# Optimization experiments

Measured on AMD Instinct MI355X. Metric: run time of the kernel, lower is better.

## Reference

```python
import jax, jax.numpy as jnp
import numpy as np

NEG = -1e9  # stand-in for -inf mask fill (avoids NaN, softmax weight ~0)
EPS = 1e-5  # torch LayerNorm default


def layer_norm(x, g, b):
    mu = jnp.mean(x, axis=-1, keepdims=True)
    var = jnp.mean(jnp.square(x - mu), axis=-1, keepdims=True)
    return (x - mu) * jax.lax.rsqrt(var + EPS) * g + b


def _forward(x, context, batch_lengths, max_len,
             Wq1, Wk1, Wv1, Wq2, Wk2, Wv2,
             ln1_g, ln1_b, ln2_g, ln2_b, ln3_g, ln3_b,
             fc1_w, fc1_b, fc2_w, fc2_b):
    B, L, E = x.shape
    H, _, dk = Wq1.shape
    pos = jnp.arange(L)
    valid = pos[None, :] < batch_lengths[:, None]                  # [B,L]
    out_mask = valid[:, :, None].astype(x.dtype)                   # [B,L,1] (outputMask)
    key_bias = jnp.where(valid, 0.0, NEG)[:, None, None, :]        # [B,1,1,L] (attnMask on keys)
    causal_bias = jnp.where(pos[:, None] >= pos[None, :], 0.0, NEG)  # [L,L] decoding mask
    scale = 1.0 / jnp.sqrt(jnp.asarray(dk, x.dtype))

    def mha(qk_src, v_src, Wq, Wk, Wv, causal):
        # Q,K from qk_src, V from v_src (faithful to Head.forward)
        m = out_mask[:, None]                                      # [B,1,L,1]
        Q = jnp.einsum('ble,hed->bhld', qk_src, Wq) * m
        K = jnp.einsum('ble,hed->bhld', qk_src, Wk) * m
        V = jnp.einsum('ble,hed->bhld', v_src, Wv) * m
        e = jnp.einsum('bhid,bhjd->bhij', Q, K) + key_bias
        if causal:
            e = e + causal_bias
        s = jax.nn.softmax(e * scale, axis=-1)
        o = jnp.einsum('bhij,bhjd->bhid', s, V)
        return o.transpose(0, 2, 1, 3).reshape(B, L, E)            # concat heads

    z = mha(x, x, Wq1, Wk1, Wv1, causal=True) * out_mask
    x1 = layer_norm(x + z, ln1_g, ln1_b)
    # cross block: Q,K from context, V from x1 (as in source)
    z = mha(context, x1, Wq2, Wk2, Wv2, causal=False) * out_mask
    x2 = layer_norm(x1 + z, ln2_g, ln2_b)
    h = jax.nn.relu(x2 @ fc1_w + fc1_b) * out_mask
    z = (h @ fc2_w + fc2_b) * out_mask
    return layer_norm(x2 + z, ln3_g, ln3_b)


def setup_inputs() -> dict:
    B, L, E, H = 8, 1024, 1024, 16
    dk = E // H
    key = jax.random.key(0)
    ks = jax.random.split(key, 16)
    w = lambda k, s: jax.random.normal(k, s, jnp.float32) * 0.02
    return {
        'x': jax.random.normal(ks[0], (B, L, E), jnp.float32),
        'context': jax.random.normal(ks[1], (B, L, E), jnp.float32),
        'batch_lengths': jax.random.randint(ks[2], (B,), 1, L + 1),
        'max_len': L,
        'Wq1': w(ks[3], (H, E, dk)), 'Wk1': w(ks[4], (H, E, dk)), 'Wv1': w(ks[5], (H, E, dk)),
        'Wq2': w(ks[6], (H, E, dk)), 'Wk2': w(ks[7], (H, E, dk)), 'Wv2': w(ks[8], (H, E, dk)),
        'ln1_g': jnp.ones((E,), jnp.float32), 'ln1_b': jnp.zeros((E,), jnp.float32),
        'ln2_g': jnp.ones((E,), jnp.float32), 'ln2_b': jnp.zeros((E,), jnp.float32),
        'ln3_g': jnp.ones((E,), jnp.float32), 'ln3_b': jnp.zeros((E,), jnp.float32),
        'fc1_w': w(ks[9], (E, E)), 'fc1_b': jnp.zeros((E,), jnp.float32),
        'fc2_w': w(ks[10], (E, E)), 'fc2_b': jnp.zeros((E,), jnp.float32),
    }


def reference(x, context, batch_lengths, max_len,
              Wq1, Wk1, Wv1, Wq2, Wk2, Wv2,
              ln1_g, ln1_b, ln2_g, ln2_b, ln3_g, ln3_b,
              fc1_w, fc1_b, fc2_w, fc2_b):
    return _forward(x, context, batch_lengths, max_len,
                    Wq1, Wk1, Wv1, Wq2, Wk2, Wv2,
                    ln1_g, ln1_b, ln2_g, ln2_b, ln3_g, ln3_b,
                    fc1_w, fc1_b, fc2_w, fc2_b)
```

## Files before the change

### kernel.cpp

```cpp
#include <hip/hip_runtime.h>


typedef unsigned short u16;
typedef unsigned int u32;
typedef __attribute__((ext_vector_type(8))) short bf16x8;
typedef __attribute__((ext_vector_type(4))) float f32x4;

#define Bv 8
#define Lv 1024
#define Ev 1024
#define Hv 16
#define DKv 64
#define Mv (Bv * Lv)

__device__ __forceinline__ u16 f2bf(float f) {
    u32 u = __float_as_uint(f);
    u += 0x7fffu + ((u >> 16) & 1u);
    return (u16)(u >> 16);
}
__device__ __forceinline__ u32 pack2(float a, float b) {
    u32 ua = __float_as_uint(a); ua += 0x7fffu + ((ua >> 16) & 1u);
    u32 ub = __float_as_uint(b); ub += 0x7fffu + ((ub >> 16) & 1u);
    return (ua >> 16) | (ub & 0xffff0000u);
}

__global__ __launch_bounds__(256) void conv_k(const float* __restrict__ s, u16* __restrict__ d) {
    int i4 = (blockIdx.x * 256 + threadIdx.x) * 4;
    float4 v = *(const float4*)(s + i4);
    uint2 o = {pack2(v.x, v.y), pack2(v.z, v.w)};
    *(uint2*)(d + i4) = o;
}

__global__ __launch_bounds__(256) void trans_attn(const float* __restrict__ s, u16* __restrict__ d) {
    __shared__ float t[32][33];
    const int d0 = blockIdx.x * 32, e0 = blockIdx.y * 32, h = blockIdx.z;
    const int tx = threadIdx.x, ty = threadIdx.y;
#pragma unroll
    for (int i = 0; i < 4; i++)
        t[ty + i * 8][tx] = s[(size_t)h * Ev * DKv + (size_t)(e0 + ty + i * 8) * DKv + d0 + tx];
    __syncthreads();
#pragma unroll
    for (int i = 0; i < 4; i++)
        d[(size_t)(h * DKv + d0 + ty + i * 8) * Ev + e0 + tx] = f2bf(t[tx][ty + i * 8]);
}

__global__ __launch_bounds__(256) void trans_fc(const float* __restrict__ s, u16* __restrict__ d) {
    __shared__ float t[32][33];
    const int n0 = blockIdx.x * 32, k0 = blockIdx.y * 32;
    const int tx = threadIdx.x, ty = threadIdx.y;
#pragma unroll
    for (int i = 0; i < 4; i++)
        t[ty + i * 8][tx] = s[(size_t)(k0 + ty + i * 8) * Ev + n0 + tx];
    __syncthreads();
#pragma unroll
    for (int i = 0; i < 4; i++)
        d[(size_t)(n0 + ty + i * 8) * Ev + k0 + tx] = f2bf(t[tx][ty + i * 8]);
}

template <int BIAS, int RELU, int TRANSOUT>
__global__ __launch_bounds__(256) void mgemm(const u16* __restrict__ A,
                                             const u16* __restrict__ Wt,
                                             const float* __restrict__ bias,
                                             u16* __restrict__ C,
                                             const int* __restrict__ lens) {
    __shared__ u16 Alds[16 * 520];
    __shared__ u16 Blds[16 * 520];
    const int tid = threadIdx.x;
    const int w = tid >> 6, l = tid & 63;
    const int lc = l & 15, lq = l >> 4;
    const int row0 = blockIdx.y * 128, col0 = blockIdx.x * 128;
    const int wm4 = (w >> 1) * 4, wn4 = (w & 1) * 4;

    f32x4 acc[4][4];
#pragma unroll
    for (int i = 0; i < 4; i++)
#pragma unroll
        for (int j = 0; j < 4; j++) acc[i][j] = (f32x4){0.f, 0.f, 0.f, 0.f};

    for (int k0 = 0; k0 < Ev; k0 += 64) {
        const u16* Ag = A + (size_t)row0 * Ev + k0;
        const u16* Bg = Wt + (size_t)col0 * Ev + k0;
#pragma unroll
        for (int i = 0; i < 4; i++) {
            int s = i * 256 + tid;
            int row = s >> 3, g = s & 7;
            uint4 va = *(const uint4*)(Ag + (size_t)row * Ev + g * 8);
            uint4 vb = *(const uint4*)(Bg + (size_t)row * Ev + g * 8);
            int off = ((row >> 4) * 2 + (g >> 2)) * 520 + ((g & 3) * 16 + (row & 15)) * 8;
            *(uint4*)(Alds + off) = va;
            *(uint4*)(Blds + off) = vb;
        }
        __syncthreads();
#pragma unroll
        for (int km = 0; km < 2; km++) {
            bf16x8 af[4], bfr[4];
#pragma unroll
            for (int mt = 0; mt < 4; mt++)
                af[mt] = *(const bf16x8*)(Alds + ((wm4 + mt) * 2 + km) * 520 + l * 8);
#pragma unroll
            for (int nt = 0; nt < 4; nt++)
                bfr[nt] = *(const bf16x8*)(Blds + ((wn4 + nt) * 2 + km) * 520 + l * 8);
#pragma unroll
            for (int mt = 0; mt < 4; mt++)
#pragma unroll
                for (int nt = 0; nt < 4; nt++)
                    acc[mt][nt] = __builtin_amdgcn_mfma_f32_16x16x32_bf16(
                        af[mt], bfr[nt], acc[mt][nt], 0, 0, 0);
        }
        __syncthreads();
    }

    int len = lens[row0 >> 10];
    len = min(max(len, 0), Lv);
    float bv[4];
#pragma unroll
    for (int nt = 0; nt < 4; nt++)
        bv[nt] = BIAS ? bias[col0 + wn4 * 16 + nt * 16 + lc] : 0.f;

#pragma unroll
    for (int mt = 0; mt < 4; mt++) {
        const int rowb = row0 + wm4 * 16 + mt * 16 + lq * 4;
#pragma unroll
        for (int nt = 0; nt < 4; nt++) {
            const int col = col0 + wn4 * 16 + nt * 16 + lc;
            float v[4];
#pragma unroll
            for (int r = 0; r < 4; r++) {
                float x = acc[mt][nt][r] + bv[nt];
                if (RELU) x = fmaxf(x, 0.f);
                v[r] = (((rowb + r) & (Lv - 1)) >= len) ? 0.f : x;
            }
            if (TRANSOUT) {
                uint2 o = {pack2(v[0], v[1]), pack2(v[2], v[3])};
                *(uint2*)(C + (size_t)col * Mv + rowb) = o;
            } else {
#pragma unroll
                for (int r = 0; r < 4; r++)
                    C[(size_t)(rowb + r) * Ev + col] = f2bf(v[r]);
            }
        }
    }
}

template <int CAUSAL>
__global__ __launch_bounds__(256) void mattn(u16* __restrict__ QZ,
                                             const u16* __restrict__ K,
                                             const u16* __restrict__ VT,
                                             const int* __restrict__ lens) {
    __shared__ u16 Kt[128 * 72];
    __shared__ u16 Vt[64 * 136];
    __shared__ u16 Pw[4 * 16 * 136];
    const int b = blockIdx.z, h = blockIdx.y, qb = blockIdx.x;
    const int q0 = qb * 64;
    const int tid = threadIdx.x;
    const int w = tid >> 6, l = tid & 63;
    const int lc = l & 15, lq = l >> 4;
    int len = lens[b];
    len = min(max(len, 0), Lv);

    if (q0 >= len) {
        const int row = q0 + (tid >> 2), cc = (tid & 3) * 16;
        uint4 z4 = {0u, 0u, 0u, 0u};
        uint4* p = (uint4*)(QZ + (size_t)(b * Lv + row) * Ev + h * DKv + cc);
        p[0] = z4; p[1] = z4;
        return;
    }

    const size_t qrow = (size_t)(b * Lv + q0 + w * 16 + lc) * Ev + h * DKv;
    bf16x8 qf[2];
    qf[0] = *(const bf16x8*)(QZ + qrow + lq * 8);
    qf[1] = *(const bf16x8*)(QZ + qrow + 32 + lq * 8);

    f32x4 of[4];
#pragma unroll
    for (int i = 0; i < 4; i++) of[i] = (f32x4){0.f, 0.f, 0.f, 0.f};
    float mrow[4] = {-1e30f, -1e30f, -1e30f, -1e30f};
    float lrow[4] = {0.f, 0.f, 0.f, 0.f};

    const int jend = CAUSAL ? min(len, q0 + 64) : len;
    const int ntiles = (jend + 127) >> 7;

    for (int kt = 0; kt < ntiles; kt++) {
        const int key0 = kt * 128;
        __syncthreads();
        {
            const u16* kg = K + (size_t)(b * Lv + key0 + (tid & 127)) * Ev + h * DKv + (tid >> 7) * 32;
            u16* kd = Kt + (tid & 127) * 72 + (tid >> 7) * 32;
#pragma unroll
            for (int c = 0; c < 4; c++) *(uint4*)(kd + c * 8) = *(const uint4*)(kg + c * 8);
            const u16* vg = VT + (size_t)(h * DKv + (tid >> 2)) * Mv + b * Lv + key0 + (tid & 3) * 32;
            u16* vd = Vt + (tid >> 2) * 136 + (tid & 3) * 32;
#pragma unroll
            for (int c = 0; c < 4; c++) *(uint4*)(vd + c * 8) = *(const uint4*)(vg + c * 8);
        }
        __syncthreads();

        f32x4 sf[8];
#pragma unroll
        for (int nt = 0; nt < 8; nt++) {
            bf16x8 b0 = *(const bf16x8*)(Kt + (nt * 16 + lc) * 72 + lq * 8);
            bf16x8 b1 = *(const bf16x8*)(Kt + (nt * 16 + lc) * 72 + 32 + lq * 8);
            f32x4 s = (f32x4){0.f, 0.f, 0.f, 0.f};
            s = __builtin_amdgcn_mfma_f32_16x16x32_bf16(qf[0], b0, s, 0, 0, 0);
            s = __builtin_amdgcn_mfma_f32_16x16x32_bf16(qf[1], b1, s, 0, 0, 0);
            sf[nt] = s;
        }
        float tmax[4] = {-1e30f, -1e30f, -1e30f, -1e30f};
#pragma unroll
        for (int nt = 0; nt < 8; nt++) {
            const int jj = key0 + nt * 16 + lc;
            const bool jv = jj < len;
#pragma unroll
            for (int r = 0; r < 4; r++) {
                const int iq = q0 + w * 16 + lq * 4 + r;
                const bool valid = jv && (!CAUSAL || jj <= iq);
                float e = valid ? sf[nt][r] * 0.125f : -1e30f;
                sf[nt][r] = e;
                tmax[r] = fmaxf(tmax[r], e);
            }
        }
#pragma unroll
        for (int r = 0; r < 4; r++) {
#pragma unroll
            for (int d = 1; d < 16; d <<= 1)
                tmax[r] = fmaxf(tmax[r], __shfl_xor(tmax[r], d, 64));
        }
        float alpha[4], mnew[4], psum[4];
#pragma unroll
        for (int r = 0; r < 4; r++) {
            mnew[r] = fmaxf(mrow[r], tmax[r]);
            alpha[r] = __expf(mrow[r] - mnew[r]);
            psum[r] = 0.f;
        }
#pragma unroll
        for (int nt = 0; nt < 8; nt++)
#pragma unroll
            for (int r = 0; r < 4; r++) {
                float p = __expf(sf[nt][r] - mnew[r]);
                sf[nt][r] = p;
                psum[r] += p;
            }
#pragma unroll
        for (int r = 0; r < 4; r++) {
#pragma unroll
            for (int d = 1; d < 16; d <<= 1) psum[r] += __shfl_xor(psum[r], d, 64);
            lrow[r] = lrow[r] * alpha[r] + psum[r];
            mrow[r] = mnew[r];
        }
#pragma unroll
        for (int nd = 0; nd < 4; nd++)
#pragma unroll
            for (int r = 0; r < 4; r++) of[nd][r] *= alpha[r];
        u16* pw = Pw + w * (16 * 136);
#pragma unroll
        for (int nt = 0; nt < 8; nt++)
#pragma unroll
            for (int r = 0; r < 4; r++)
                pw[(lq * 4 + r) * 136 + nt * 16 + lc] = f2bf(sf[nt][r]);
#pragma unroll
        for (int nd = 0; nd < 4; nd++) {
#pragma unroll
            for (int km = 0; km < 4; km++) {
                bf16x8 pa = *(const bf16x8*)(pw + lc * 136 + km * 32 + lq * 8);
                bf16x8 vb = *(const bf16x8*)(Vt + (nd * 16 + lc) * 136 + km * 32 + lq * 8);
                of[nd] = __builtin_amdgcn_mfma_f32_16x16x32_bf16(pa, vb, of[nd], 0, 0, 0);
            }
        }
    }

    float inv[4];
#pragma unroll
    for (int r = 0; r < 4; r++) {
        const int iq = q0 + w * 16 + lq * 4 + r;
        inv[r] = (iq < len && lrow[r] > 0.f) ? (1.f / lrow[r]) : 0.f;
    }
#pragma unroll
    for (int nd = 0; nd < 4; nd++)
#pragma unroll
        for (int r = 0; r < 4; r++)
            QZ[(size_t)(b * Lv + q0 + w * 16 + lq * 4 + r) * Ev + h * DKv + nd * 16 + lc] =
                f2bf(of[nd][r] * inv[r]);
}

__device__ __forceinline__ float bf_lo(u32 u) { return __uint_as_float(u << 16); }
__device__ __forceinline__ float bf_hi(u32 u) { return __uint_as_float(u & 0xffff0000u); }

template <int BASEBF, int OUTF32>
__global__ __launch_bounds__(256) void ln_k(const void* __restrict__ base,
                                            const u16* __restrict__ z,
                                            const float* __restrict__ g,
                                            const float* __restrict__ bta,
                                            void* __restrict__ out) {
    __shared__ float r1[256], r2[256];
    const int row = blockIdx.x, t = threadIdx.x;
    const int c0 = t * 4;
    float v[4];
    if (BASEBF) {
        uint2 bu = *(const uint2*)((const u16*)base + (size_t)row * Ev + c0);
        v[0] = bf_lo(bu.x); v[1] = bf_hi(bu.x); v[2] = bf_lo(bu.y); v[3] = bf_hi(bu.y);
    } else {
        float4 f = *(const float4*)((const float*)base + (size_t)row * Ev + c0);
        v[0] = f.x; v[1] = f.y; v[2] = f.z; v[3] = f.w;
    }
    uint2 zu = *(const uint2*)(z + (size_t)row * Ev + c0);
    v[0] += bf_lo(zu.x); v[1] += bf_hi(zu.x); v[2] += bf_lo(zu.y); v[3] += bf_hi(zu.y);
    r1[t] = v[0] + v[1] + v[2] + v[3];
    r2[t] = v[0] * v[0] + v[1] * v[1] + v[2] * v[2] + v[3] * v[3];
    __syncthreads();
    for (int s = 128; s > 0; s >>= 1) {
        if (t < s) { r1[t] += r1[t + s]; r2[t] += r2[t + s]; }
        __syncthreads();
    }
    const float mu = r1[0] * (1.f / Ev);
    const float var = r2[0] * (1.f / Ev) - mu * mu;
    const float rinv = rsqrtf(fmaxf(var, 0.f) + 1e-5f);
    float4 gv = *(const float4*)(g + c0);
    float4 bv = *(const float4*)(bta + c0);
    float y[4];
    y[0] = (v[0] - mu) * rinv * gv.x + bv.x;
    y[1] = (v[1] - mu) * rinv * gv.y + bv.y;
    y[2] = (v[2] - mu) * rinv * gv.z + bv.z;
    y[3] = (v[3] - mu) * rinv * gv.w + bv.w;
    if (OUTF32) {
        float4 ow = {y[0], y[1], y[2], y[3]};
        *(float4*)((float*)out + (size_t)row * Ev + c0) = ow;
    } else {
        uint2 ow = {pack2(y[0], y[1]), pack2(y[2], y[3])};
        *(uint2*)((u16*)out + (size_t)row * Ev + c0) = ow;
    }
}

extern "C" void kernel_launch(void* const* d_in, const int* in_sizes, int n_in,
                              void* d_out, int out_size, void* d_ws, size_t ws_size,
                              hipStream_t stream) {
    const float* x    = (const float*)d_in[0];
    const float* ctx  = (const float*)d_in[1];
    const int*   lens = (const int*)d_in[2];
    const float* Wq1 = (const float*)d_in[4];
    const float* Wk1 = (const float*)d_in[5];
    const float* Wv1 = (const float*)d_in[6];
    const float* Wq2 = (const float*)d_in[7];
    const float* Wk2 = (const float*)d_in[8];
    const float* Wv2 = (const float*)d_in[9];
    const float* g1 = (const float*)d_in[10], *b1 = (const float*)d_in[11];
    const float* g2 = (const float*)d_in[12], *b2 = (const float*)d_in[13];
    const float* g3 = (const float*)d_in[14], *b3 = (const float*)d_in[15];
    const float* fc1w = (const float*)d_in[16], *fc1b = (const float*)d_in[17];
    const float* fc2w = (const float*)d_in[18], *fc2b = (const float*)d_in[19];

    const size_t WSZ = (size_t)Ev * Ev;
    const size_t MM  = (size_t)Mv * Ev;
    u16* WT = (u16*)d_ws;
    u16* Wtq1 = WT + 0 * WSZ, *Wtk1 = WT + 1 * WSZ, *Wtv1 = WT + 2 * WSZ;
    u16* Wtq2 = WT + 3 * WSZ, *Wtk2 = WT + 4 * WSZ, *Wtv2 = WT + 5 * WSZ;
    u16* Wtf1 = WT + 6 * WSZ, *Wtf2 = WT + 7 * WSZ;
    u16* B1 = WT + 8 * WSZ;
    u16* B2 = B1 + MM;
    u16* B3 = B2 + MM;
    u16* B4 = B3 + MM;
    u16* xb = (u16*)d_out;
    u16* cb = xb + MM;

    dim3 gC(Mv * Ev / 1024), gTA(2, 32, Hv), gTF(32, 32), bT(32, 8);
    dim3 gG(8, 64), gA(16, Hv, Bv), gL(Mv);

    conv_k<<<gC, 256, 0, stream>>>(x, xb);
    conv_k<<<gC, 256, 0, stream>>>(ctx, cb);
    trans_attn<<<gTA, bT, 0, stream>>>(Wq1, Wtq1);
    trans_attn<<<gTA, bT, 0, stream>>>(Wk1, Wtk1);
    trans_attn<<<gTA, bT, 0, stream>>>(Wv1, Wtv1);
    trans_attn<<<gTA, bT, 0, stream>>>(Wq2, Wtq2);
    trans_attn<<<gTA, bT, 0, stream>>>(Wk2, Wtk2);
    trans_attn<<<gTA, bT, 0, stream>>>(Wv2, Wtv2);
    trans_fc<<<gTF, bT, 0, stream>>>(fc1w, Wtf1);
    trans_fc<<<gTF, bT, 0, stream>>>(fc2w, Wtf2);

    mgemm<0, 0, 0><<<gG, 256, 0, stream>>>(xb, Wtq1, nullptr, B1, lens);
    mgemm<0, 0, 0><<<gG, 256, 0, stream>>>(xb, Wtk1, nullptr, B2, lens);
    mgemm<0, 0, 1><<<gG, 256, 0, stream>>>(xb, Wtv1, nullptr, B3, lens);
    mattn<1><<<gA, 256, 0, stream>>>(B1, B2, B3, lens);
    ln_k<0, 0><<<gL, 256, 0, stream>>>(x, B1, g1, b1, B2);

    mgemm<0, 0, 0><<<gG, 256, 0, stream>>>(cb, Wtq2, nullptr, B1, lens);
    mgemm<0, 0, 0><<<gG, 256, 0, stream>>>(cb, Wtk2, nullptr, B3, lens);
    mgemm<0, 0, 1><<<gG, 256, 0, stream>>>(B2, Wtv2, nullptr, B4, lens);
    mattn<0><<<gA, 256, 0, stream>>>(B1, B3, B4, lens);
    ln_k<1, 0><<<gL, 256, 0, stream>>>(B2, B1, g2, b2, B3);

    mgemm<1, 1, 0><<<gG, 256, 0, stream>>>(B3, Wtf1, fc1b, B1, lens);
    mgemm<1, 0, 0><<<gG, 256, 0, stream>>>(B1, Wtf2, fc2b, B4, lens);
    ln_k<1, 1><<<gL, 256, 0, stream>>>(B3, B4, g3, b3, d_out);
}
```

Before: 566.7 us.

## Fuse QKV projections, use direct global-to-LDS loads, enlarge attention query tile

```diff
diff --git a/kernel.cpp b/kernel.cpp
--- a/kernel.cpp
+++ b/kernel.cpp
@@ -13,6 +13,24 @@
 #define DKv 64
 #define Mv (Bv * Lv)
 
+#if defined(__has_builtin)
+# if __has_builtin(__builtin_amdgcn_global_load_lds)
+#  define HAS_GLL 1
+# endif
+#endif
+#ifndef HAS_GLL
+# define HAS_GLL 0
+#endif
+
+#if HAS_GLL
+__device__ __forceinline__ void gll16(const u16* g, u16* l) {
+    __builtin_amdgcn_global_load_lds(
+        (const __attribute__((address_space(1))) void*)(unsigned long long)(g),
+        (__attribute__((address_space(3))) void*)(unsigned)(unsigned long long)(l),
+        16, 0, 0);
+}
+#endif
+
 __device__ __forceinline__ u16 f2bf(float f) {
     u32 u = __float_as_uint(f);
     u += 0x7fffu + ((u >> 16) & 1u);
@@ -23,6 +41,8 @@
     u32 ub = __float_as_uint(b); ub += 0x7fffu + ((ub >> 16) & 1u);
     return (ua >> 16) | (ub & 0xffff0000u);
 }
+__device__ __forceinline__ float bf_lo(u32 u) { return __uint_as_float(u << 16); }
+__device__ __forceinline__ float bf_hi(u32 u) { return __uint_as_float(u & 0xffff0000u); }
 
 __global__ __launch_bounds__(256) void conv_k(const float* __restrict__ s, u16* __restrict__ d) {
     int i4 = (blockIdx.x * 256 + threadIdx.x) * 4;
@@ -57,18 +77,21 @@
         d[(size_t)(n0 + ty + i * 8) * Ev + k0 + tx] = f2bf(t[tx][ty + i * 8]);
 }
 
-template <int BIAS, int RELU, int TRANSOUT>
+template <int BIAS, int RELU, int TRANSW>
 __global__ __launch_bounds__(256) void mgemm(const u16* __restrict__ A,
                                              const u16* __restrict__ Wt,
                                              const float* __restrict__ bias,
-                                             u16* __restrict__ C,
+                                             u16* __restrict__ O0, u16* __restrict__ O1,
+                                             u16* __restrict__ O2,
                                              const int* __restrict__ lens) {
-    __shared__ u16 Alds[16 * 520];
-    __shared__ u16 Blds[16 * 520];
+    __shared__ u16 Alds[16 * 512];
+    __shared__ u16 Blds[16 * 512];
     const int tid = threadIdx.x;
     const int w = tid >> 6, l = tid & 63;
     const int lc = l & 15, lq = l >> 4;
     const int row0 = blockIdx.y * 128, col0 = blockIdx.x * 128;
+    const int which = col0 >> 10, colL = col0 & 1023;
+    u16* C = (which == 0) ? O0 : (which == 1 ? O1 : O2);
     const int wm4 = (w >> 1) * 4, wn4 = (w & 1) * 4;
 
     f32x4 acc[4][4];
@@ -77,29 +100,39 @@
 #pragma unroll
         for (int j = 0; j < 4; j++) acc[i][j] = (f32x4){0.f, 0.f, 0.f, 0.f};
 
+    const u16* Ag[4]; const u16* Bg[4]; u16* Al[4]; u16* Bl[4];
+#pragma unroll
+    for (int i = 0; i < 4; i++) {
+        const int g16 = 2 * w + (i >> 1), k32 = i & 1;
+        Ag[i] = A  + (size_t)(row0 + g16 * 16 + lc) * Ev + k32 * 32 + lq * 8;
+        Bg[i] = Wt + (size_t)(col0 + g16 * 16 + lc) * Ev + k32 * 32 + lq * 8;
+        Al[i] = Alds + (g16 * 2 + k32) * 512;
+        Bl[i] = Blds + (g16 * 2 + k32) * 512;
+    }
+
     for (int k0 = 0; k0 < Ev; k0 += 64) {
-        const u16* Ag = A + (size_t)row0 * Ev + k0;
-        const u16* Bg = Wt + (size_t)col0 * Ev + k0;
+#if HAS_GLL
+#pragma unroll
+        for (int i = 0; i < 4; i++) { gll16(Ag[i], Al[i]); gll16(Bg[i], Bl[i]); }
+#else
 #pragma unroll
         for (int i = 0; i < 4; i++) {
-            int s = i * 256 + tid;
-            int row = s >> 3, g = s & 7;
-            uint4 va = *(const uint4*)(Ag + (size_t)row * Ev + g * 8);
-            uint4 vb = *(const uint4*)(Bg + (size_t)row * Ev + g * 8);
-            int off = ((row >> 4) * 2 + (g >> 2)) * 520 + ((g & 3) * 16 + (row & 15)) * 8;
-            *(uint4*)(Alds + off) = va;
-            *(uint4*)(Blds + off) = vb;
-        }
+            *(uint4*)(Al[i] + l * 8) = *(const uint4*)Ag[i];
+            *(uint4*)(Bl[i] + l * 8) = *(const uint4*)Bg[i];
+        }
+#endif
+#pragma unroll
+        for (int i = 0; i < 4; i++) { Ag[i] += 64; Bg[i] += 64; }
         __syncthreads();
 #pragma unroll
         for (int km = 0; km < 2; km++) {
             bf16x8 af[4], bfr[4];
 #pragma unroll
             for (int mt = 0; mt < 4; mt++)
-                af[mt] = *(const bf16x8*)(Alds + ((wm4 + mt) * 2 + km) * 520 + l * 8);
+                af[mt] = *(const bf16x8*)(Alds + ((wm4 + mt) * 2 + km) * 512 + l * 8);
 #pragma unroll
             for (int nt = 0; nt < 4; nt++)
-                bfr[nt] = *(const bf16x8*)(Blds + ((wn4 + nt) * 2 + km) * 520 + l * 8);
+                bfr[nt] = *(const bf16x8*)(Blds + ((wn4 + nt) * 2 + km) * 512 + l * 8);
 #pragma unroll
             for (int mt = 0; mt < 4; mt++)
 #pragma unroll
@@ -112,17 +145,18 @@
 
     int len = lens[row0 >> 10];
     len = min(max(len, 0), Lv);
+    const bool tr = (TRANSW == which);
     float bv[4];
 #pragma unroll
     for (int nt = 0; nt < 4; nt++)
-        bv[nt] = BIAS ? bias[col0 + wn4 * 16 + nt * 16 + lc] : 0.f;
+        bv[nt] = BIAS ? bias[colL + wn4 * 16 + nt * 16 + lc] : 0.f;
 
 #pragma unroll
     for (int mt = 0; mt < 4; mt++) {
         const int rowb = row0 + wm4 * 16 + mt * 16 + lq * 4;
 #pragma unroll
         for (int nt = 0; nt < 4; nt++) {
-            const int col = col0 + wn4 * 16 + nt * 16 + lc;
+            const int col = colL + wn4 * 16 + nt * 16 + lc;
             float v[4];
 #pragma unroll
             for (int r = 0; r < 4; r++) {
@@ -130,7 +164,7 @@
                 if (RELU) x = fmaxf(x, 0.f);
                 v[r] = (((rowb + r) & (Lv - 1)) >= len) ? 0.f : x;
             }
-            if (TRANSOUT) {
+            if (tr) {
                 uint2 o = {pack2(v[0], v[1]), pack2(v[2], v[3])};
                 *(uint2*)(C + (size_t)col * Mv + rowb) = o;
             } else {
@@ -147,11 +181,11 @@
                                              const u16* __restrict__ K,
                                              const u16* __restrict__ VT,
                                              const int* __restrict__ lens) {
-    __shared__ u16 Kt[128 * 72];
-    __shared__ u16 Vt[64 * 136];
-    __shared__ u16 Pw[4 * 16 * 136];
+    __shared__ u16 Kt[16 * 512];
+    __shared__ u16 Vt[16 * 512];
+    __shared__ u16 Pt[4 * 4 * 512];
     const int b = blockIdx.z, h = blockIdx.y, qb = blockIdx.x;
-    const int q0 = qb * 64;
+    const int q0 = qb * 128;
     const int tid = threadIdx.x;
     const int w = tid >> 6, l = tid & 63;
     const int lc = l & 15, lq = l >> 4;
@@ -159,131 +193,166 @@
     len = min(max(len, 0), Lv);
 
     if (q0 >= len) {
-        const int row = q0 + (tid >> 2), cc = (tid & 3) * 16;
+        const int zr = tid >> 1, zc = (tid & 1) * 32;
         uint4 z4 = {0u, 0u, 0u, 0u};
-        uint4* p = (uint4*)(QZ + (size_t)(b * Lv + row) * Ev + h * DKv + cc);
-        p[0] = z4; p[1] = z4;
+        uint4* p = (uint4*)(QZ + (size_t)(b * Lv + q0 + zr) * Ev + h * DKv + zc);
+        p[0] = z4; p[1] = z4; p[2] = z4; p[3] = z4;
         return;
     }
 
-    const size_t qrow = (size_t)(b * Lv + q0 + w * 16 + lc) * Ev + h * DKv;
-    bf16x8 qf[2];
-    qf[0] = *(const bf16x8*)(QZ + qrow + lq * 8);
-    qf[1] = *(const bf16x8*)(QZ + qrow + 32 + lq * 8);
-
-    f32x4 of[4];
-#pragma unroll
-    for (int i = 0; i < 4; i++) of[i] = (f32x4){0.f, 0.f, 0.f, 0.f};
-    float mrow[4] = {-1e30f, -1e30f, -1e30f, -1e30f};
-    float lrow[4] = {0.f, 0.f, 0.f, 0.f};
-
-    const int jend = CAUSAL ? min(len, q0 + 64) : len;
+    bf16x8 qf[2][2];
+#pragma unroll
+    for (int mt = 0; mt < 2; mt++)
+#pragma unroll
+        for (int k2 = 0; k2 < 2; k2++)
+            qf[mt][k2] = *(const bf16x8*)(QZ + (size_t)(b * Lv + q0 + w * 32 + mt * 16 + lc) * Ev +
+                                          h * DKv + k2 * 32 + lq * 8);
+
+    f32x4 of[2][4];
+#pragma unroll
+    for (int mt = 0; mt < 2; mt++)
+#pragma unroll
+        for (int nd = 0; nd < 4; nd++) of[mt][nd] = (f32x4){0.f, 0.f, 0.f, 0.f};
+    float mrow[2][4], lrow[2][4];
+#pragma unroll
+    for (int mt = 0; mt < 2; mt++)
+#pragma unroll
+        for (int r = 0; r < 4; r++) { mrow[mt][r] = -1e30f; lrow[mt][r] = 0.f; }
+
+    const u16* Kg[4]; const u16* Vg[4]; u16* Kl[4]; u16* Vl[4];
+#pragma unroll
+    for (int i = 0; i < 4; i++) {
+        const int k16 = 2 * w + (i >> 1), d32 = i & 1;
+        Kg[i] = K + (size_t)(b * Lv + k16 * 16 + lc) * Ev + h * DKv + d32 * 32 + lq * 8;
+        Kl[i] = Kt + (k16 * 2 + d32) * 512;
+        Vg[i] = VT + (size_t)(h * DKv + w * 16 + lc) * Mv + b * Lv + i * 32 + lq * 8;
+        Vl[i] = Vt + (w * 4 + i) * 512;
+    }
+    u16* Pw = Pt + w * 2048;
+
+    const int jend = CAUSAL ? min(len, q0 + 128) : len;
     const int ntiles = (jend + 127) >> 7;
 
     for (int kt = 0; kt < ntiles; kt++) {
-        const int key0 = kt * 128;
+        const int koff = kt * 128;
+#if HAS_GLL
+#pragma unroll
+        for (int i = 0; i < 4; i++) {
+            gll16(Kg[i] + (size_t)koff * Ev, Kl[i]);
+            gll16(Vg[i] + koff, Vl[i]);
+        }
+#else
+#pragma unroll
+        for (int i = 0; i < 4; i++) {
+            *(uint4*)(Kl[i] + l * 8) = *(const uint4*)(Kg[i] + (size_t)koff * Ev);
+            *(uint4*)(Vl[i] + l * 8) = *(const uint4*)(Vg[i] + koff);
+        }
+#endif
         __syncthreads();
-        {
-            const u16* kg = K + (size_t)(b * Lv + key0 + (tid & 127)) * Ev + h * DKv + (tid >> 7) * 32;
-            u16* kd = Kt + (tid & 127) * 72 + (tid >> 7) * 32;
-#pragma unroll
-            for (int c = 0; c < 4; c++) *(uint4*)(kd + c * 8) = *(const uint4*)(kg + c * 8);
-            const u16* vg = VT + (size_t)(h * DKv + (tid >> 2)) * Mv + b * Lv + key0 + (tid & 3) * 32;
-            u16* vd = Vt + (tid >> 2) * 136 + (tid & 3) * 32;
-#pragma unroll
-            for (int c = 0; c < 4; c++) *(uint4*)(vd + c * 8) = *(const uint4*)(vg + c * 8);
+
+        f32x4 sf[2][8];
+#pragma unroll
+        for (int nt = 0; nt < 8; nt++) {
+            bf16x8 kf0 = *(const bf16x8*)(Kt + (nt * 2 + 0) * 512 + l * 8);
+            bf16x8 kf1 = *(const bf16x8*)(Kt + (nt * 2 + 1) * 512 + l * 8);
+#pragma unroll
+            for (int mt = 0; mt < 2; mt++) {
+                f32x4 s = (f32x4){0.f, 0.f, 0.f, 0.f};
+                s = __builtin_amdgcn_mfma_f32_16x16x32_bf16(qf[mt][0], kf0, s, 0, 0, 0);
+                s = __builtin_amdgcn_mfma_f32_16x16x32_bf16(qf[mt][1], kf1, s, 0, 0, 0);
+                sf[mt][nt] = s;
+            }
+        }
+
+        float alpha[2][4];
+#pragma unroll
+        for (int mt = 0; mt < 2; mt++) {
+            float tmax[4] = {-1e30f, -1e30f, -1e30f, -1e30f};
+#pragma unroll
+            for (int nt = 0; nt < 8; nt++) {
+                const int jj = koff + nt * 16 + lc;
+                const bool jv = jj < len;
+#pragma unroll
+                for (int r = 0; r < 4; r++) {
+                    const int iq = q0 + w * 32 + mt * 16 + lq * 4 + r;
+                    const bool valid = jv && (!CAUSAL || jj <= iq);
+                    float e = valid ? sf[mt][nt][r] * 0.125f : -1e30f;
+                    sf[mt][nt][r] = e;
+                    tmax[r] = fmaxf(tmax[r], e);
+                }
+            }
+#pragma unroll
+            for (int r = 0; r < 4; r++) {
+#pragma unroll
+                for (int d = 1; d < 16; d <<= 1)
+                    tmax[r] = fmaxf(tmax[r], __shfl_xor(tmax[r], d, 64));
+            }
+            float psum[4];
+#pragma unroll
+            for (int r = 0; r < 4; r++) {
+                const float mn = fmaxf(mrow[mt][r], tmax[r]);
+                alpha[mt][r] = __expf(mrow[mt][r] - mn);
+                mrow[mt][r] = mn;
+                psum[r] = 0.f;
+            }
+#pragma unroll
+            for (int nt = 0; nt < 8; nt++)
+#pragma unroll
+                for (int r = 0; r < 4; r++) {
+                    float p = __expf(sf[mt][nt][r] - mrow[mt][r]);
+                    sf[mt][nt][r] = p;
+                    psum[r] += p;
+                }
+#pragma unroll
+            for (int r = 0; r < 4; r++) {
+#pragma unroll
+                for (int d = 1; d < 16; d <<= 1) psum[r] += __shfl_xor(psum[r], d, 64);
+                lrow[mt][r] = lrow[mt][r] * alpha[mt][r] + psum[r];
+            }
+#pragma unroll
+            for (int nd = 0; nd < 4; nd++)
+#pragma unroll
+                for (int r = 0; r < 4; r++) of[mt][nd][r] *= alpha[mt][r];
+        }
+
+#pragma unroll
+        for (int mt = 0; mt < 2; mt++) {
+#pragma unroll
+            for (int nt = 0; nt < 8; nt++)
+#pragma unroll
+                for (int r = 0; r < 4; r++)
+                    Pw[(nt >> 1) * 512 +
+                       ((2 * (nt & 1) + (lc >> 3)) * 16 + lq * 4 + r) * 8 + (lc & 7)] =
+                        f2bf(sf[mt][nt][r]);
+#pragma unroll
+            for (int km = 0; km < 4; km++) {
+                bf16x8 pa = *(const bf16x8*)(Pw + km * 512 + l * 8);
+#pragma unroll
+                for (int nd = 0; nd < 4; nd++) {
+                    bf16x8 vb = *(const bf16x8*)(Vt + (nd * 4 + km) * 512 + l * 8);
+                    of[mt][nd] = __builtin_amdgcn_mfma_f32_16x16x32_bf16(pa, vb, of[mt][nd], 0, 0, 0);
+                }
+            }
         }
         __syncthreads();
-
-        f32x4 sf[8];
-#pragma unroll
-        for (int nt = 0; nt < 8; nt++) {
-            bf16x8 b0 = *(const bf16x8*)(Kt + (nt * 16 + lc) * 72 + lq * 8);
-            bf16x8 b1 = *(const bf16x8*)(Kt + (nt * 16 + lc) * 72 + 32 + lq * 8);
-            f32x4 s = (f32x4){0.f, 0.f, 0.f, 0.f};
-            s = __builtin_amdgcn_mfma_f32_16x16x32_bf16(qf[0], b0, s, 0, 0, 0);
-            s = __builtin_amdgcn_mfma_f32_16x16x32_bf16(qf[1], b1, s, 0, 0, 0);
-            sf[nt] = s;
-        }
-        float tmax[4] = {-1e30f, -1e30f, -1e30f, -1e30f};
-#pragma unroll
-        for (int nt = 0; nt < 8; nt++) {
-            const int jj = key0 + nt * 16 + lc;
-            const bool jv = jj < len;
-#pragma unroll
-            for (int r = 0; r < 4; r++) {
-                const int iq = q0 + w * 16 + lq * 4 + r;
-                const bool valid = jv && (!CAUSAL || jj <= iq);
-                float e = valid ? sf[nt][r] * 0.125f : -1e30f;
-                sf[nt][r] = e;
-                tmax[r] = fmaxf(tmax[r], e);
-            }
-        }
+    }
+
+#pragma unroll
+    for (int mt = 0; mt < 2; mt++) {
+        float inv[4];
 #pragma unroll
         for (int r = 0; r < 4; r++) {
-#pragma unroll
-            for (int d = 1; d < 16; d <<= 1)
-                tmax[r] = fmaxf(tmax[r], __shfl_xor(tmax[r], d, 64));
-        }
-        float alpha[4], mnew[4], psum[4];
-#pragma unroll
-        for (int r = 0; r < 4; r++) {
-            mnew[r] = fmaxf(mrow[r], tmax[r]);
-            alpha[r] = __expf(mrow[r] - mnew[r]);
-            psum[r] = 0.f;
-        }
-#pragma unroll
-        for (int nt = 0; nt < 8; nt++)
-#pragma unroll
-            for (int r = 0; r < 4; r++) {
-                float p = __expf(sf[nt][r] - mnew[r]);
-                sf[nt][r] = p;
-                psum[r] += p;
-            }
-#pragma unroll
-        for (int r = 0; r < 4; r++) {
-#pragma unroll
-            for (int d = 1; d < 16; d <<= 1) psum[r] += __shfl_xor(psum[r], d, 64);
-            lrow[r] = lrow[r] * alpha[r] + psum[r];
-            mrow[r] = mnew[r];
+            const int iq = q0 + w * 32 + mt * 16 + lq * 4 + r;
+            inv[r] = (iq < len && lrow[mt][r] > 0.f) ? (1.f / lrow[mt][r]) : 0.f;
         }
 #pragma unroll
         for (int nd = 0; nd < 4; nd++)
 #pragma unroll
-            for (int r = 0; r < 4; r++) of[nd][r] *= alpha[r];
-        u16* pw = Pw + w * (16 * 136);
-#pragma unroll
-        for (int nt = 0; nt < 8; nt++)
-#pragma unroll
             for (int r = 0; r < 4; r++)
-                pw[(lq * 4 + r) * 136 + nt * 16 + lc] = f2bf(sf[nt][r]);
-#pragma unroll
-        for (int nd = 0; nd < 4; nd++) {
-#pragma unroll
-            for (int km = 0; km < 4; km++) {
-                bf16x8 pa = *(const bf16x8*)(pw + lc * 136 + km * 32 + lq * 8);
-                bf16x8 vb = *(const bf16x8*)(Vt + (nd * 16 + lc) * 136 + km * 32 + lq * 8);
-                of[nd] = __builtin_amdgcn_mfma_f32_16x16x32_bf16(pa, vb, of[nd], 0, 0, 0);
-            }
-        }
-    }
-
-    float inv[4];
-#pragma unroll
-    for (int r = 0; r < 4; r++) {
-        const int iq = q0 + w * 16 + lq * 4 + r;
-        inv[r] = (iq < len && lrow[r] > 0.f) ? (1.f / lrow[r]) : 0.f;
-    }
-#pragma unroll
-    for (int nd = 0; nd < 4; nd++)
-#pragma unroll
-        for (int r = 0; r < 4; r++)
-            QZ[(size_t)(b * Lv + q0 + w * 16 + lq * 4 + r) * Ev + h * DKv + nd * 16 + lc] =
-                f2bf(of[nd][r] * inv[r]);
-}
-
-__device__ __forceinline__ float bf_lo(u32 u) { return __uint_as_float(u << 16); }
-__device__ __forceinline__ float bf_hi(u32 u) { return __uint_as_float(u & 0xffff0000u); }
+                QZ[(size_t)(b * Lv + q0 + w * 32 + mt * 16 + lq * 4 + r) * Ev +
+                   h * DKv + nd * 16 + lc] = f2bf(of[mt][nd][r] * inv[r]);
+    }
+}
 
 template <int BASEBF, int OUTF32>
 __global__ __launch_bounds__(256) void ln_k(const void* __restrict__ base,
@@ -362,7 +431,7 @@
     u16* cb = xb + MM;
 
     dim3 gC(Mv * Ev / 1024), gTA(2, 32, Hv), gTF(32, 32), bT(32, 8);
-    dim3 gG(8, 64), gA(16, Hv, Bv), gL(Mv);
+    dim3 gQKV(24, 64), gQK(16, 64), gG1(8, 64), gA(8, Hv, Bv), gL(Mv);
 
     conv_k<<<gC, 256, 0, stream>>>(x, xb);
     conv_k<<<gC, 256, 0, stream>>>(ctx, cb);
@@ -375,19 +444,16 @@
     trans_fc<<<gTF, bT, 0, stream>>>(fc1w, Wtf1);
     trans_fc<<<gTF, bT, 0, stream>>>(fc2w, Wtf2);
 
-    mgemm<0, 0, 0><<<gG, 256, 0, stream>>>(xb, Wtq1, nullptr, B1, lens);
-    mgemm<0, 0, 0><<<gG, 256, 0, stream>>>(xb, Wtk1, nullptr, B2, lens);
-    mgemm<0, 0, 1><<<gG, 256, 0, stream>>>(xb, Wtv1, nullptr, B3, lens);
+    mgemm<0, 0, 2><<<gQKV, 256, 0, stream>>>(xb, Wtq1, nullptr, B1, B2, B3, lens);
     mattn<1><<<gA, 256, 0, stream>>>(B1, B2, B3, lens);
     ln_k<0, 0><<<gL, 256, 0, stream>>>(x, B1, g1, b1, B2);
 
-    mgemm<0, 0, 0><<<gG, 256, 0, stream>>>(cb, Wtq2, nullptr, B1, lens);
-    mgemm<0, 0, 0><<<gG, 256, 0, stream>>>(cb, Wtk2, nullptr, B3, lens);
-    mgemm<0, 0, 1><<<gG, 256, 0, stream>>>(B2, Wtv2, nullptr, B4, lens);
+    mgemm<0, 0, -1><<<gQK, 256, 0, stream>>>(cb, Wtq2, nullptr, B1, B3, nullptr, lens);
+    mgemm<0, 0, 0><<<gG1, 256, 0, stream>>>(B2, Wtv2, nullptr, B4, nullptr, nullptr, lens);
     mattn<0><<<gA, 256, 0, stream>>>(B1, B3, B4, lens);
     ln_k<1, 0><<<gL, 256, 0, stream>>>(B2, B1, g2, b2, B3);
 
-    mgemm<1, 1, 0><<<gG, 256, 0, stream>>>(B3, Wtf1, fc1b, B1, lens);
-    mgemm<1, 0, 0><<<gG, 256, 0, stream>>>(B1, Wtf2, fc2b, B4, lens);
-    ln_k<1, 1><<<gL, 256, 0, stream>>>(B3, B4, g3, b3, d_out);
-}
+    mgemm<1, 1, -1><<<gG1, 256, 0, stream>>>(B3, Wtf1, fc1b, B1, nullptr, nullptr, lens);
+    mgemm<1, 0, -1><<<gG1, 256, 0, stream>>>(B1, Wtf2, fc2b, B2, nullptr, nullptr, lens);
+    ln_k<1, 1><<<gL, 256, 0, stream>>>(B3, B2, g3, b3, d_out);
+}
```

After: 602.0 us. +6.2%, slower.
